# Kernel optimization log

Measured on AMD Instinct MI355X. Metric: run time of the kernel, lower is better.

The kernel has to match this reference:

```python
import jax, jax.numpy as jnp
import numpy as np
from jax import lax

H = 512  # hidden_size
L = 2    # num_layers


def _lstm_scan(xs, h0, c0, Wih, Whh, bih, bhh):
    """PyTorch-convention LSTM over full sequence.
    xs: [B,T,D]; h0,c0: [B,H]; Wih: [4H,D]; Whh: [4H,H].
    Gate order i,f,g,o. Returns (outputs [B,T,H], hT, cT)."""
    WihT = Wih.T
    WhhT = Whh.T
    b = bih + bhh

    def step(carry, xt):
        h, c = carry
        g = xt @ WihT + h @ WhhT + b          # [B,4H]
        i, f, gg, o = jnp.split(g, 4, axis=-1)
        i = jax.nn.sigmoid(i)
        f = jax.nn.sigmoid(f)
        gg = jnp.tanh(gg)
        o = jax.nn.sigmoid(o)
        c = f * c + i * gg
        h = o * jnp.tanh(c)
        return (h, c), h

    (hT, cT), hs = lax.scan(step, (h0, c0), jnp.swapaxes(xs, 0, 1))
    return jnp.swapaxes(hs, 0, 1), hT, cT


def setup_inputs() -> dict:
    key = jax.random.key(0)
    ks = jax.random.split(key, 24)
    B, T, I = 128, 512, 128
    s = 0.05  # small init scale, like 1/sqrt(H)
    inp = {
        "x": jax.random.normal(ks[0], (B, T, I), jnp.float32),
        "c_dec": jax.random.uniform(ks[1], (L, B, H), jnp.float32),  # torch.rand_like(hx)
    }
    names = [
        ("enc_Wih0", (4 * H, I)), ("enc_Whh0", (4 * H, H)), ("enc_bih0", (4 * H,)), ("enc_bhh0", (4 * H,)),
        ("enc_Wih1", (4 * H, H)), ("enc_Whh1", (4 * H, H)), ("enc_bih1", (4 * H,)), ("enc_bhh1", (4 * H,)),
        ("dec_Wih0", (4 * H, I)), ("dec_Whh0", (4 * H, H)), ("dec_bih0", (4 * H,)), ("dec_bhh0", (4 * H,)),
        ("dec_Wih1", (4 * H, H)), ("dec_Whh1", (4 * H, H)), ("dec_bih1", (4 * H,)), ("dec_bhh1", (4 * H,)),
        ("fc_W", (I, H)), ("fc_b", (I,)),
    ]
    for j, (name, shape) in enumerate(names):
        inp[name] = jax.random.normal(ks[2 + j], shape, jnp.float32) * s
    return inp


def reference(x, c_dec,
              enc_Wih0, enc_Whh0, enc_bih0, enc_bhh0,
              enc_Wih1, enc_Whh1, enc_bih1, enc_bhh1,
              dec_Wih0, dec_Whh0, dec_bih0, dec_bhh0,
              dec_Wih1, dec_Whh1, dec_bih1, dec_bhh1,
              fc_W, fc_b):
    B = x.shape[0]
    z = jnp.zeros((B, H), x.dtype)
    # ---- encoder: 2-layer LSTM, zero init; keep final hidden per layer ----
    e0, h0T, _ = _lstm_scan(x, z, z, enc_Wih0, enc_Whh0, enc_bih0, enc_bhh0)
    _, h1T, _ = _lstm_scan(e0, z, z, enc_Wih1, enc_Whh1, enc_bih1, enc_bhh1)
    # ---- decoder with teacher forcing: input seq is [0, x_0, ..., x_{T-2}] ----
    dec_in = jnp.concatenate([jnp.zeros_like(x[:, :1]), x[:, :-1]], axis=1)
    d0, _, _ = _lstm_scan(dec_in, h0T, c_dec[0], dec_Wih0, dec_Whh0, dec_bih0, dec_bhh0)
    d1, _, _ = _lstm_scan(d0, h1T, c_dec[1], dec_Wih1, dec_Whh1, dec_bih1, dec_bhh1)
    # FC head on top-layer hidden states -> decoder_sequence [B,T,I]
    return d1 @ fc_W.T + fc_b
```

## Files before the change

kernel.cpp:

```cpp
#include <hip/hip_runtime.h>
#include <stdint.h>


using bf16x8 = __attribute__((ext_vector_type(8))) short;
using u32x4  = __attribute__((ext_vector_type(4))) uint32_t;
using f32x16 = __attribute__((ext_vector_type(16))) float;
using f32x4  = __attribute__((ext_vector_type(4))) float;

#define MFMA32(a, b, c) __builtin_amdgcn_mfma_f32_32x32x16_bf16((a), (b), (c), 0, 0, 0)
#define MFMA16(a, b, c) __builtin_amdgcn_mfma_f32_16x16x32_bf16((a), (b), (c), 0, 0, 0)

static __device__ __forceinline__ uint16_t f2bf(float f) {
  union { float f; uint32_t u; } v; v.f = f;
  uint32_t u = v.u;
  return (uint16_t)((u + 0x7fffu + ((u >> 16) & 1u)) >> 16);
}
static __device__ __forceinline__ float sigm(float x) { return 1.0f / (1.0f + __expf(-x)); }
static __device__ __forceinline__ float tanh_f(float x) { return 2.0f / (1.0f + __expf(-2.0f * x)) - 1.0f; }

static __device__ __forceinline__ bf16x8 cvt8(const float* p) {
  bf16x8 r;
#pragma unroll
  for (int i = 0; i < 8; ++i) { uint16_t b = f2bf(p[i]); r[i] = (short)b; }
  return r;
}

static __device__ __forceinline__ uint32_t aldf(const uint32_t* p) {
  return __hip_atomic_load(p, __ATOMIC_RELAXED, __HIP_MEMORY_SCOPE_AGENT);
}
static __device__ __forceinline__ void ldg16(bf16x8& d, const uint16_t* p) {
  asm volatile("global_load_dwordx4 %0, %1, off sc0 sc1" : "=v"(d) : "v"(p) : "memory");
}
static __device__ __forceinline__ void stg16(uint16_t* p, u32x4 v) {
  asm volatile("global_store_dwordx4 %0, %1, off sc0 sc1" :: "v"(p), "v"(v) : "memory");
}

static const size_t OFF_FLG = 0;
static const size_t OFF_HB0 = 1024;
static const size_t OFF_HB1 = 1024 + 1048576;

__global__ void init_kernel(uint32_t* flg, uint32_t* h0a, uint32_t* h0b) {
  int i = (int)blockIdx.x * 256 + (int)threadIdx.x;
  if (i < 256) flg[i] = 0;
  for (int j = i; j < 32768; j += (int)gridDim.x * 256) { h0a[j] = 0; h0b[j] = 0; }
}

struct PJob {
  const float* whh;
  const float* wih;
  const float* bih;
  const float* bhh;
  const float* xf;
  const uint16_t* xring;
  uint16_t* hring;
  const float* c0;
  uint32_t* fown;
  const uint32_t* fprod;
  const uint32_t* fcons;
  const float* fcw;
  const float* fcb;
  const uint16_t* fchr;
  float* out;
  int KX;
  int shift;
  int tsteps;
  uint32_t fb;
};

__global__ void __launch_bounds__(256, 1) lstm_pipe(PJob j0, PJob j1) {
  const PJob J = ((int)blockIdx.x < 128) ? j0 : j1;
  const int lb = (int)blockIdx.x & 127;
  const int bg = lb >> 6, u = lb & 63, b0 = bg * 64;
  const int tid = (int)threadIdx.x;
  const int wv = tid >> 6, ln = tid & 63;

  __shared__ __align__(16) uint16_t Wl[40960];
  __shared__ float gb[2][64][33];
  __shared__ float cst[64][9];
  __shared__ __align__(16) uint32_t hst[64][4];

  const int KX = J.KX;
  const int NTX = KX >> 5;
  const int HS = (16 + NTX) * 512;

  {
    const int nfrag = (2 * HS) >> 3;
    for (int f = tid; f < nfrag; f += 256) {
      int lane = f & 63;
      int kt2 = f >> 6;
      int kh = (kt2 >= 16 + NTX) ? 1 : 0;
      int kt = kt2 - kh * (16 + NTX);
      int col = lane & 31;
      int wrow = ((col >> 3) << 9) + (u << 3) + (col & 7);
      int m = (kt << 4) + ((lane >> 5) << 3);
      const float* src = (m < 256)
          ? J.whh + (size_t)wrow * 512 + (kh << 8) + m
          : J.wih + (size_t)wrow * KX + kh * (KX >> 1) + (m - 256);
      union { uint16_t h[8]; ulonglong2 v; } tmp;
#pragma unroll
      for (int j = 0; j < 8; ++j) tmp.h[j] = f2bf(src[j]);
      *(ulonglong2*)(Wl + (size_t)f * 8) = tmp.v;
    }
  }

  const int isfc = (J.fcw != nullptr) && (u < 8);
  const int wgti = bg * 8 + u;
  const int ftc = wgti & 7;
  const int ftr = 2 * wv + (wgti >> 3);
  const int fcol = ftc * 16 + (ln & 15);
  const int farow = ftr * 16 + (ln & 15);
  float fbv = 0.0f;
  if (isfc) {
    fbv = J.fcb[fcol];
    for (int f = tid; f < 1024; f += 256) {
      int lane = f & 63, kt = f >> 6;
      int row = ftc * 16 + (lane & 15);
      int k = (kt << 5) + ((lane >> 4) << 3);
      const float* src = J.fcw + (size_t)row * 512 + k;
      union { uint16_t h[8]; ulonglong2 v; } tmp;
#pragma unroll
      for (int j = 0; j < 8; ++j) tmp.h[j] = f2bf(src[j]);
      *(ulonglong2*)(Wl + 32768 + (size_t)f * 8) = tmp.v;
    }
  }

  const int rl = tid >> 2, ul2 = (tid & 3) * 2, bE = b0 + rl;
  const int hu = u * 8 + ul2;
  const float Bi0 = J.bih[hu] + J.bhh[hu];
  const float Bi1 = J.bih[hu + 1] + J.bhh[hu + 1];
  const float Bf0 = J.bih[512 + hu] + J.bhh[512 + hu];
  const float Bf1 = J.bih[513 + hu] + J.bhh[513 + hu];
  const float Bg0 = J.bih[1024 + hu] + J.bhh[1024 + hu];
  const float Bg1 = J.bih[1025 + hu] + J.bhh[1025 + hu];
  const float Bo0 = J.bih[1536 + hu] + J.bhh[1536 + hu];
  const float Bo1 = J.bih[1537 + hu] + J.bhh[1537 + hu];
  {
    float c0v = 0.f, c1v = 0.f;
    if (J.c0) {
      c0v = J.c0[(size_t)bE * 512 + hu];
      c1v = J.c0[(size_t)bE * 512 + hu + 1];
    }
    cst[rl][ul2] = c0v;
    cst[rl][ul2 + 1] = c1v;
  }
  __syncthreads();

  const int mt = wv & 1, kh = wv >> 1;
  const int arow = b0 + mt * 32 + (ln & 31);
  const size_t hbase = (size_t)arow * 512 + (size_t)kh * 256 + ((ln >> 5) << 3);
  const uint16_t* wlh = Wl + (size_t)kh * HS + (size_t)ln * 8;
  const uint16_t* wlx = wlh + 16 * 512;
  const int tsteps = J.tsteps;
  const uint32_t FB = J.fb;

  for (int t = 0; t < tsteps; ++t) {
    f32x16 acc;
#pragma unroll
    for (int r = 0; r < 16; ++r) acc[r] = 0.0f;

    if (t < 512 && J.xring == nullptr) {
      const int tx = t - J.shift;
      if (tx >= 0) {
        const float* xb = J.xf + (size_t)arow * (512 * (size_t)KX) +
                          (size_t)tx * KX + kh * (KX >> 1) + ((ln >> 5) << 3);
        for (int kt = 0; kt < NTX; ++kt) {
          bf16x8 af = cvt8(xb + kt * 16);
          acc = MFMA32(af, *(const bf16x8*)(wlx + kt * 512), acc);
        }
      }
    }

    if (wv == 0) {
      const uint32_t* po = J.fown + bg * 64;
      const uint32_t* pp = J.fprod ? J.fprod + bg * 64 : nullptr;
      const uint32_t* pc = J.fcons ? J.fcons + bg * 64 : nullptr;
      const uint32_t* pf = J.fcons;
      const int w_own  = (t >= 1) && (t < 512);
      const int w_prod = (pp != nullptr) && (t < 512);
      const int w_cons = (pc != nullptr) && (t >= 8) && (t < 512);
      const int w_fc   = isfc && (t >= 4);
      if (w_own | w_prod | w_cons | w_fc) {
        const uint32_t to  = FB + (uint32_t)t;
        const uint32_t tp  = to + 1u;
        const uint32_t tcn = to - 7u;
        const uint32_t tfc = to - 3u;
        while (1) {
          int ok = 1;
          if (w_own)  ok &= (aldf(po + ln) >= to);
          if (w_prod) ok &= (aldf(pp + ln) >= tp);
          if (w_cons) ok &= (aldf(pc + ln) >= tcn);
          if (w_fc) {
            ok &= (aldf(pf + ln) >= tfc);
            ok &= (aldf(pf + 64 + ln) >= tfc);
          }
          if (__all(ok)) break;
          __builtin_amdgcn_s_sleep(1);
        }
      }
    }
    __syncthreads();

    if (t < 512) {
      const uint16_t* hb = J.hring + (size_t)(t & 7) * 65536 + hbase;
      bf16x8 ah[16];
#pragma unroll
      for (int kt = 0; kt < 16; ++kt) ldg16(ah[kt], hb + kt * 16);
      if (J.xring) {
        const uint16_t* xb = J.xring + (size_t)((t + 1) & 7) * 65536 + hbase;
        bf16x8 ax[16];
#pragma unroll
        for (int kt = 0; kt < 16; ++kt) ldg16(ax[kt], xb + kt * 16);
        asm volatile("s_waitcnt vmcnt(0)" ::: "memory");
        __builtin_amdgcn_sched_barrier(0);
#pragma unroll
        for (int kt = 0; kt < 16; ++kt)
          acc = MFMA32(ah[kt], *(const bf16x8*)(wlh + kt * 512), acc);
#pragma unroll
        for (int kt = 0; kt < 16; ++kt)
          acc = MFMA32(ax[kt], *(const bf16x8*)(wlx + kt * 512), acc);
      } else {
        asm volatile("s_waitcnt vmcnt(0)" ::: "memory");
        __builtin_amdgcn_sched_barrier(0);
#pragma unroll
        for (int kt = 0; kt < 16; ++kt)
          acc = MFMA32(ah[kt], *(const bf16x8*)(wlh + kt * 512), acc);
      }
#pragma unroll
      for (int r = 0; r < 16; ++r) {
        int crow = (r & 3) + 8 * (r >> 2) + 4 * (ln >> 5);
        gb[kh][mt * 32 + crow][ln & 31] = acc[r];
      }
      __syncthreads();

      float i0 = sigm(gb[0][rl][ul2]      + gb[1][rl][ul2]      + Bi0);
      float i1 = sigm(gb[0][rl][ul2 + 1]  + gb[1][rl][ul2 + 1]  + Bi1);
      float f0 = sigm(gb[0][rl][8 + ul2]  + gb[1][rl][8 + ul2]  + Bf0);
      float f1 = sigm(gb[0][rl][9 + ul2]  + gb[1][rl][9 + ul2]  + Bf1);
      float g0 = tanh_f(gb[0][rl][16 + ul2] + gb[1][rl][16 + ul2] + Bg0);
      float g1 = tanh_f(gb[0][rl][17 + ul2] + gb[1][rl][17 + ul2] + Bg1);
      float o0 = sigm(gb[0][rl][24 + ul2] + gb[1][rl][24 + ul2] + Bo0);
      float o1 = sigm(gb[0][rl][25 + ul2] + gb[1][rl][25 + ul2] + Bo1);
      float cc0 = f0 * cst[rl][ul2]     + i0 * g0;
      float cc1 = f1 * cst[rl][ul2 + 1] + i1 * g1;
      cst[rl][ul2] = cc0;
      cst[rl][ul2 + 1] = cc1;
      float h0 = o0 * tanh_f(cc0);
      float h1 = o1 * tanh_f(cc1);
      hst[rl][ul2 >> 1] = (uint32_t)f2bf(h0) | ((uint32_t)f2bf(h1) << 16);

      __syncthreads();

      if (wv == 0) {
        u32x4 hv4;
#pragma unroll
        for (int q = 0; q < 4; ++q) hv4[q] = hst[ln][q];
        uint16_t* dst = J.hring + (size_t)((t + 1) & 7) * 65536 +
                        (size_t)(b0 + ln) * 512 + (size_t)(u << 3);
        stg16(dst, hv4);
        asm volatile("s_waitcnt vmcnt(0)" ::: "memory");
        if (ln == 0)
          __hip_atomic_store(J.fown + bg * 64 + u, FB + (uint32_t)(t + 1),
                             __ATOMIC_RELAXED, __HIP_MEMORY_SCOPE_AGENT);
      }
    }

    if (isfc && t >= 4) {
      const int tf = t - 4;
      const uint16_t* ha = J.fchr + (size_t)((tf + 1) & 7) * 65536 +
                           (size_t)farow * 512 + ((ln >> 4) << 3);
      const uint16_t* wb = Wl + 32768 + (size_t)ln * 8;
      bf16x8 af[16];
#pragma unroll
      for (int kt = 0; kt < 16; ++kt) ldg16(af[kt], ha + kt * 32);
      asm volatile("s_waitcnt vmcnt(0)" ::: "memory");
      __builtin_amdgcn_sched_barrier(0);
      f32x4 fa;
      fa[0] = fa[1] = fa[2] = fa[3] = 0.0f;
#pragma unroll
      for (int kt = 0; kt < 16; ++kt)
        fa = MFMA16(af[kt], *(const bf16x8*)(wb + kt * 512), fa);
#pragma unroll
      for (int r = 0; r < 4; ++r) {
        int row = ftr * 16 + ((ln >> 4) << 2) + r;
        J.out[((size_t)row * 512 + tf) * 128 + fcol] = fa[r] + fbv;
      }
    }
  }
}

extern "C" void kernel_launch(void* const* d_in, const int* in_sizes, int n_in,
                              void* d_out, int out_size, void* d_ws, size_t ws_size,
                              hipStream_t stream) {
  (void)in_sizes; (void)n_in; (void)out_size; (void)ws_size;
  uint8_t* ws = (uint8_t*)d_ws;
  const float* x     = (const float*)d_in[0];
  const float* c_dec = (const float*)d_in[1];
  const float* W[16];
  for (int i = 0; i < 16; ++i) W[i] = (const float*)d_in[2 + i];
  const float* fcW = (const float*)d_in[18];
  const float* fcb = (const float*)d_in[19];

  uint32_t* FLG = (uint32_t*)(ws + OFF_FLG);
  uint16_t* HB0 = (uint16_t*)(ws + OFF_HB0);
  uint16_t* HB1 = (uint16_t*)(ws + OFF_HB1);
  uint32_t* FL0 = FLG + 0;
  uint32_t* FL1 = FLG + 128;

  hipLaunchKernelGGL(init_kernel, dim3(128), dim3(256), 0, stream,
                     FLG, (uint32_t*)HB0, (uint32_t*)HB1);

  {
    PJob a; a.whh = W[1]; a.wih = W[0]; a.bih = W[2]; a.bhh = W[3];
    a.xf = x; a.xring = nullptr; a.hring = HB0; a.c0 = nullptr;
    a.fown = FL0; a.fprod = nullptr; a.fcons = FL1;
    a.fcw = nullptr; a.fcb = nullptr; a.fchr = nullptr; a.out = nullptr;
    a.KX = 128; a.shift = 0; a.tsteps = 512; a.fb = 0;
    PJob b; b.whh = W[5]; b.wih = W[4]; b.bih = W[6]; b.bhh = W[7];
    b.xf = nullptr; b.xring = HB0; b.hring = HB1; b.c0 = nullptr;
    b.fown = FL1; b.fprod = FL0; b.fcons = nullptr;
    b.fcw = nullptr; b.fcb = nullptr; b.fchr = nullptr; b.out = nullptr;
    b.KX = 512; b.shift = 0; b.tsteps = 512; b.fb = 0;
    void* args[2] = { &a, &b };
    (void)hipLaunchCooperativeKernel((const void*)lstm_pipe, dim3(256), dim3(256), args, 0, stream);
  }

  {
    PJob a; a.whh = W[9]; a.wih = W[8]; a.bih = W[10]; a.bhh = W[11];
    a.xf = x; a.xring = nullptr; a.hring = HB0; a.c0 = c_dec;
    a.fown = FL0; a.fprod = nullptr; a.fcons = FL1;
    a.fcw = fcW; a.fcb = fcb; a.fchr = HB1; a.out = (float*)d_out;
    a.KX = 128; a.shift = 1; a.tsteps = 516; a.fb = 512;
    PJob b; b.whh = W[13]; b.wih = W[12]; b.bih = W[14]; b.bhh = W[15];
    b.xf = nullptr; b.xring = HB0; b.hring = HB1; b.c0 = c_dec + 65536;
    b.fown = FL1; b.fprod = FL0; b.fcons = nullptr;
    b.fcw = nullptr; b.fcb = nullptr; b.fchr = nullptr; b.out = nullptr;
    b.KX = 512; b.shift = 0; b.tsteps = 512; b.fb = 512;
    void* args[2] = { &a, &b };
    (void)hipLaunchCooperativeKernel((const void*)lstm_pipe, dim3(256), dim3(256), args, 0, stream);
  }
}
```

Baseline: 8.697 ms.

## Enlarge hidden-state rings and use L2-cached loads with periodic acquire invalidation

Grows the hidden-state ring buffers from 8 slots up to 32 or 64, depending on workspace size. The h/x ring reads drop the sc1 bit so they can hit in L2 instead of going to coherent memory. Stale-cache hazards are handled with staggered periodic acquire loads, which invalidate caches every (P-8) steps, and a consumer back-pressure window widened to match the ring size. This aims to cut global-load latency on the per-step recurrent critical path. The trade-off is more fragile memory-ordering correctness, and the choice of path now depends on ws_size.

```diff
diff --git a/kernel.cpp b/kernel.cpp
--- a/kernel.cpp
+++ b/kernel.cpp
@@ -28,21 +28,34 @@
 static __device__ __forceinline__ uint32_t aldf(const uint32_t* p) {
   return __hip_atomic_load(p, __ATOMIC_RELAXED, __HIP_MEMORY_SCOPE_AGENT);
 }
+static __device__ __forceinline__ void ldg16_c(bf16x8& d, const uint16_t* p) {
+  asm volatile("global_load_dwordx4 %0, %1, off sc0" : "=v"(d) : "v"(p) : "memory");
+}
+static __device__ __forceinline__ void ldg16_u(bf16x8& d, const uint16_t* p) {
+  asm volatile("global_load_dwordx4 %0, %1, off sc0 sc1" : "=v"(d) : "v"(p) : "memory");
+}
+template <int C>
 static __device__ __forceinline__ void ldg16(bf16x8& d, const uint16_t* p) {
-  asm volatile("global_load_dwordx4 %0, %1, off sc0 sc1" : "=v"(d) : "v"(p) : "memory");
+  if (C) ldg16_c(d, p); else ldg16_u(d, p);
 }
 static __device__ __forceinline__ void stg16(uint16_t* p, u32x4 v) {
   asm volatile("global_store_dwordx4 %0, %1, off sc0 sc1" :: "v"(p), "v"(v) : "memory");
 }
-
-static const size_t OFF_FLG = 0;
-static const size_t OFF_HB0 = 1024;
-static const size_t OFF_HB1 = 1024 + 1048576;
+static __device__ __forceinline__ void stgf(float* p, float v) {
+  asm volatile("global_store_dword %0, %1, off sc0 sc1" :: "v"(p), "v"(v) : "memory");
+}
+static __device__ __forceinline__ void l2_acquire(const uint32_t* p) {
+  (void)__hip_atomic_load(p, __ATOMIC_ACQUIRE, __HIP_MEMORY_SCOPE_AGENT);
+}
+
 
 __global__ void init_kernel(uint32_t* flg, uint32_t* h0a, uint32_t* h0b) {
   int i = (int)blockIdx.x * 256 + (int)threadIdx.x;
-  if (i < 256) flg[i] = 0;
-  for (int j = i; j < 32768; j += (int)gridDim.x * 256) { h0a[j] = 0; h0b[j] = 0; }
+  if (i < 256) __hip_atomic_store(flg + i, 0u, __ATOMIC_RELAXED, __HIP_MEMORY_SCOPE_AGENT);
+  for (int j = i; j < 32768; j += (int)gridDim.x * 256) {
+    __hip_atomic_store(h0a + j, 0u, __ATOMIC_RELAXED, __HIP_MEMORY_SCOPE_AGENT);
+    __hip_atomic_store(h0b + j, 0u, __ATOMIC_RELAXED, __HIP_MEMORY_SCOPE_AGENT);
+  }
 }
 
 struct PJob {
@@ -65,8 +78,11 @@
   int shift;
   int tsteps;
   uint32_t fb;
+  int pm;
+  int ivp;
 };
 
+template <int CACHED>
 __global__ void __launch_bounds__(256, 1) lstm_pipe(PJob j0, PJob j1) {
   const PJob J = ((int)blockIdx.x < 128) ? j0 : j1;
   const int lb = (int)blockIdx.x & 127;
@@ -152,6 +168,8 @@
   const uint16_t* wlx = wlh + 16 * 512;
   const int tsteps = J.tsteps;
   const uint32_t FB = J.fb;
+  const int pm = J.pm;
+  const int PP = pm + 1;
 
   for (int t = 0; t < tsteps; ++t) {
     f32x16 acc;
@@ -177,12 +195,12 @@
       const uint32_t* pf = J.fcons;
       const int w_own  = (t >= 1) && (t < 512);
       const int w_prod = (pp != nullptr) && (t < 512);
-      const int w_cons = (pc != nullptr) && (t >= 8) && (t < 512);
+      const int w_cons = (pc != nullptr) && (t >= PP) && (t < 512);
       const int w_fc   = isfc && (t >= 4);
       if (w_own | w_prod | w_cons | w_fc) {
         const uint32_t to  = FB + (uint32_t)t;
         const uint32_t tp  = to + 1u;
-        const uint32_t tcn = to - 7u;
+        const uint32_t tcn = to - (uint32_t)(PP - 1);
         const uint32_t tfc = to - 3u;
         while (1) {
           int ok = 1;
@@ -200,16 +218,22 @@
     }
     __syncthreads();
 
+    if (CACHED) {
+      if ((t == 0) || (((uint32_t)(t + u * 5) % (uint32_t)J.ivp) == 0)) {
+        l2_acquire(J.fown + bg * 64 + u);
+      }
+    }
+
     if (t < 512) {
-      const uint16_t* hb = J.hring + (size_t)(t & 7) * 65536 + hbase;
+      const uint16_t* hb = J.hring + (size_t)(t & pm) * 65536 + hbase;
       bf16x8 ah[16];
 #pragma unroll
-      for (int kt = 0; kt < 16; ++kt) ldg16(ah[kt], hb + kt * 16);
+      for (int kt = 0; kt < 16; ++kt) ldg16<CACHED>(ah[kt], hb + kt * 16);
       if (J.xring) {
-        const uint16_t* xb = J.xring + (size_t)((t + 1) & 7) * 65536 + hbase;
+        const uint16_t* xb = J.xring + (size_t)((t + 1) & pm) * 65536 + hbase;
         bf16x8 ax[16];
 #pragma unroll
-        for (int kt = 0; kt < 16; ++kt) ldg16(ax[kt], xb + kt * 16);
+        for (int kt = 0; kt < 16; ++kt) ldg16<CACHED>(ax[kt], xb + kt * 16);
         asm volatile("s_waitcnt vmcnt(0)" ::: "memory");
         __builtin_amdgcn_sched_barrier(0);
 #pragma unroll
@@ -254,7 +278,7 @@
         u32x4 hv4;
 #pragma unroll
         for (int q = 0; q < 4; ++q) hv4[q] = hst[ln][q];
-        uint16_t* dst = J.hring + (size_t)((t + 1) & 7) * 65536 +
+        uint16_t* dst = J.hring + (size_t)((t + 1) & pm) * 65536 +
                         (size_t)(b0 + ln) * 512 + (size_t)(u << 3);
         stg16(dst, hv4);
         asm volatile("s_waitcnt vmcnt(0)" ::: "memory");
@@ -266,12 +290,12 @@
 
     if (isfc && t >= 4) {
       const int tf = t - 4;
-      const uint16_t* ha = J.fchr + (size_t)((tf + 1) & 7) * 65536 +
+      const uint16_t* ha = J.fchr + (size_t)((tf + 1) & pm) * 65536 +
                            (size_t)farow * 512 + ((ln >> 4) << 3);
       const uint16_t* wb = Wl + 32768 + (size_t)ln * 8;
       bf16x8 af[16];
 #pragma unroll
-      for (int kt = 0; kt < 16; ++kt) ldg16(af[kt], ha + kt * 32);
+      for (int kt = 0; kt < 16; ++kt) ldg16<CACHED>(af[kt], ha + kt * 32);
       asm volatile("s_waitcnt vmcnt(0)" ::: "memory");
       __builtin_amdgcn_sched_barrier(0);
       f32x4 fa;
@@ -282,7 +306,7 @@
 #pragma unroll
       for (int r = 0; r < 4; ++r) {
         int row = ftr * 16 + ((ln >> 4) << 2) + r;
-        J.out[((size_t)row * 512 + tf) * 128 + fcol] = fa[r] + fbv;
+        stgf(&J.out[((size_t)row * 512 + tf) * 128 + fcol], fa[r] + fbv);
       }
     }
   }
@@ -291,7 +315,7 @@
 extern "C" void kernel_launch(void* const* d_in, const int* in_sizes, int n_in,
                               void* d_out, int out_size, void* d_ws, size_t ws_size,
                               hipStream_t stream) {
-  (void)in_sizes; (void)n_in; (void)out_size; (void)ws_size;
+  (void)in_sizes; (void)n_in; (void)out_size;
   uint8_t* ws = (uint8_t*)d_ws;
   const float* x     = (const float*)d_in[0];
   const float* c_dec = (const float*)d_in[1];
@@ -300,11 +324,19 @@
   const float* fcW = (const float*)d_in[18];
   const float* fcb = (const float*)d_in[19];
 
-  uint32_t* FLG = (uint32_t*)(ws + OFF_FLG);
-  uint16_t* HB0 = (uint16_t*)(ws + OFF_HB0);
-  uint16_t* HB1 = (uint16_t*)(ws + OFF_HB1);
+  int P, cached;
+  if (ws_size >= 1024 + 2ull * 64 * 131072) { P = 64; cached = 1; }
+  else if (ws_size >= 1024 + 2ull * 32 * 131072) { P = 32; cached = 1; }
+  else { P = 8; cached = 0; }
+  const int IP = P - 8;
+
+  uint32_t* FLG = (uint32_t*)(ws + 0);
+  uint16_t* HB0 = (uint16_t*)(ws + 1024);
+  uint16_t* HB1 = (uint16_t*)(ws + 1024 + (size_t)P * 131072);
   uint32_t* FL0 = FLG + 0;
   uint32_t* FL1 = FLG + 128;
+
+  const void* kern = cached ? (const void*)lstm_pipe<1> : (const void*)lstm_pipe<0>;
 
   hipLaunchKernelGGL(init_kernel, dim3(128), dim3(256), 0, stream,
                      FLG, (uint32_t*)HB0, (uint32_t*)HB1);
@@ -314,14 +346,14 @@
     a.xf = x; a.xring = nullptr; a.hring = HB0; a.c0 = nullptr;
     a.fown = FL0; a.fprod = nullptr; a.fcons = FL1;
     a.fcw = nullptr; a.fcb = nullptr; a.fchr = nullptr; a.out = nullptr;
-    a.KX = 128; a.shift = 0; a.tsteps = 512; a.fb = 0;
+    a.KX = 128; a.shift = 0; a.tsteps = 512; a.fb = 0; a.pm = P - 1; a.ivp = IP;
     PJob b; b.whh = W[5]; b.wih = W[4]; b.bih = W[6]; b.bhh = W[7];
     b.xf = nullptr; b.xring = HB0; b.hring = HB1; b.c0 = nullptr;
     b.fown = FL1; b.fprod = FL0; b.fcons = nullptr;
     b.fcw = nullptr; b.fcb = nullptr; b.fchr = nullptr; b.out = nullptr;
-    b.KX = 512; b.shift = 0; b.tsteps = 512; b.fb = 0;
+    b.KX = 512; b.shift = 0; b.tsteps = 512; b.fb = 0; b.pm = P - 1; b.ivp = IP;
     void* args[2] = { &a, &b };
-    (void)hipLaunchCooperativeKernel((const void*)lstm_pipe, dim3(256), dim3(256), args, 0, stream);
+    (void)hipLaunchCooperativeKernel(kern, dim3(256), dim3(256), args, 0, stream);
   }
 
   {
@@ -329,13 +361,13 @@
     a.xf = x; a.xring = nullptr; a.hring = HB0; a.c0 = c_dec;
     a.fown = FL0; a.fprod = nullptr; a.fcons = FL1;
     a.fcw = fcW; a.fcb = fcb; a.fchr = HB1; a.out = (float*)d_out;
-    a.KX = 128; a.shift = 1; a.tsteps = 516; a.fb = 512;
+    a.KX = 128; a.shift = 1; a.tsteps = 516; a.fb = 512; a.pm = P - 1; a.ivp = IP;
     PJob b; b.whh = W[13]; b.wih = W[12]; b.bih = W[14]; b.bhh = W[15];
     b.xf = nullptr; b.xring = HB0; b.hring = HB1; b.c0 = c_dec + 65536;
     b.fown = FL1; b.fprod = FL0; b.fcons = nullptr;
     b.fcw = nullptr; b.fcb = nullptr; b.fchr = nullptr; b.out = nullptr;
-    b.KX = 512; b.shift = 0; b.tsteps = 512; b.fb = 512;
+    b.KX = 512; b.shift = 0; b.tsteps = 512; b.fb = 512; b.pm = P - 1; b.ivp = IP;
     void* args[2] = { &a, &b };
-    (void)hipLaunchCooperativeKernel((const void*)lstm_pipe, dim3(256), dim3(256), args, 0, stream);
-  }
-}
+    (void)hipLaunchCooperativeKernel(kern, dim3(256), dim3(256), args, 0, stream);
+  }
+}
```

Measured after the change: 8.428 ms. 3.1% less time.
